# Optimization experiments

Measured on AMD Instinct MI355X. Metric: run time of the kernel, lower is better.

The kernel has to match this reference:

```python
import jax, jax.numpy as jnp
import numpy as np

VOCAB = 100000
EMB = 100
HID = 100
CTX_LEN = 60          # must equal MAX_DESC_LEN for linear_1 to fit
FACT_LEN = 20
DESC_LEN = 60


def setup_inputs() -> dict:
    key = jax.random.key(0)
    ks = jax.random.split(key, 12)
    s = 0.05
    context = jax.random.randint(ks[0], (CTX_LEN, FACT_LEN), 1, VOCAB)
    fact_lengths = jax.random.randint(ks[1], (CTX_LEN,), 1, FACT_LEN)
    description = jax.random.randint(ks[2], (DESC_LEN,), 1, VOCAB)
    emb_ctx = jax.random.normal(ks[3], (VOCAB, EMB), jnp.float32) * s
    emb_ctx = emb_ctx.at[0].set(0.0)  # padding_idx=0
    emb_dec = jax.random.normal(ks[4], (VOCAB, EMB), jnp.float32) * s
    emb_dec = emb_dec.at[0].set(0.0)
    w1 = jax.random.normal(ks[5], (HID, CTX_LEN * HID), jnp.float32) * s
    b1 = jax.random.normal(ks[6], (HID,), jnp.float32) * s
    w_ih = jax.random.normal(ks[7], (3 * HID, EMB), jnp.float32) * s
    w_hh = jax.random.normal(ks[8], (3 * HID, HID), jnp.float32) * s
    b_ih = jax.random.normal(ks[9], (3 * HID,), jnp.float32) * s
    b_hh = jax.random.normal(ks[10], (3 * HID,), jnp.float32) * s
    w_out = jax.random.normal(ks[11], (VOCAB, HID), jnp.float32) * s
    b_out = jnp.zeros((VOCAB,), jnp.float32)
    return {"context": context, "fact_lengths": fact_lengths, "description": description,
            "emb_ctx": emb_ctx, "emb_dec": emb_dec, "w1": w1, "b1": b1,
            "w_ih": w_ih, "w_hh": w_hh, "b_ih": b_ih, "b_hh": b_hh,
            "w_out": w_out, "b_out": b_out}


def _forward(context, description, emb_ctx, emb_dec, w1, b1,
             w_ih, w_hh, b_ih, b_hh, w_out, b_out):
    # ---- InputModule: embed + positional fact encoder ----
    emb = emb_ctx[context]                       # [CTX_LEN, FACT_LEN, EMB]
    slen, elen = FACT_LEN, EMB
    s = jnp.arange(slen, dtype=jnp.float32) / (slen - 1)   # [slen]
    e = jnp.arange(elen, dtype=jnp.float32) / (elen - 1)   # [elen]
    l = 1.0 - s[:, None] - e[None, :] * (1.0 - 2.0 * s[:, None])  # [slen, elen]
    facts = jnp.sum(emb * l[None], axis=1)       # [CTX_LEN, EMB]

    # ---- initial decoder hidden from flattened facts ----
    h0 = facts.reshape(1, -1) @ w1.T + b1        # [1, HID]

    x0 = emb_dec[1][None, :]                     # SOS token embedding [1, EMB]

    def step(carry, tok):
        h, x = carry
        gi = x @ w_ih.T + b_ih                   # [1, 3H]
        gh = h @ w_hh.T + b_hh
        i_r, i_z, i_n = jnp.split(gi, 3, axis=-1)
        h_r, h_z, h_n = jnp.split(gh, 3, axis=-1)
        r = jax.nn.sigmoid(i_r + h_r)
        z = jax.nn.sigmoid(i_z + h_z)
        n = jnp.tanh(i_n + r * h_n)
        h_new = (1.0 - z) * n + z * h            # [1, HID]
        logits = h_new @ w_out.T + b_out         # [1, VOCAB]
        logp = jax.nn.log_softmax(logits, axis=-1)
        loss_t = -logp[0, tok]                   # NLLLoss, batch 1
        x_next = emb_dec[tok][None, :]           # teacher forcing
        return (h_new, x_next), loss_t

    (_, _), losses = jax.lax.scan(step, (h0, x0), description)
    return jnp.sum(losses).reshape(1)            # matches torch FloatTensor([.])


def reference(context, fact_lengths, description, emb_ctx, emb_dec, w1, b1,
              w_ih, w_hh, b_ih, b_hh, w_out, b_out):
    # fact_lengths is unused by the original forward (PositionalFactEncoder ignores it)
    return _forward(context, description, emb_ctx, emb_dec, w1, b1,
                    w_ih, w_hh, b_ih, b_hh, w_out, b_out)
```

## Files before the change

kernel.cpp:

```cpp
#include <hip/hip_runtime.h>
#include <hip/hip_bf16.h>
#include <math.h>

#define VOCAB 100000
#define EMB 100
#define HID 100
#define CTX_LEN 60
#define FACT_LEN 20
#define DESC_LEN 60

#define WS_FACTS 0
#define WS_X     6000
#define WS_H0    12000
#define WS_GI    12160
#define WS_H     30160
#define WS_MS    36864
#define NWAVES   1024

typedef __attribute__((ext_vector_type(8))) short short8;
typedef __attribute__((ext_vector_type(4))) float f32x4;

static __device__ __forceinline__ unsigned short f2bf(float f) {
    union { float f; unsigned u; } x; x.f = f;
    unsigned r = (x.u + 0x7FFFu + ((x.u >> 16) & 1u)) >> 16;
    return (unsigned short)r;
}

__global__ __launch_bounds__(128) void k1_prep(const int* __restrict__ context,
                                               const int* __restrict__ desc,
                                               const float* __restrict__ emb_ctx,
                                               const float* __restrict__ emb_dec,
                                               float* __restrict__ ws,
                                               float* __restrict__ out) {
    int b = blockIdx.x, tid = threadIdx.x;
    if (b < 60) {
        __shared__ int toks[20];
        if (tid < 20) toks[tid] = context[b * 20 + tid];
        __syncthreads();
        if (tid < 100) {
            float ef = tid * (1.f / 99.f);
            float acc = 0.f;
            #pragma unroll
            for (int s = 0; s < 20; s++) {
                float sf = s * (1.f / 19.f);
                float l = 1.f - sf - ef * (1.f - 2.f * sf);
                acc = fmaf(emb_ctx[toks[s] * 100 + tid], l, acc);
            }
            ws[WS_FACTS + b * 100 + tid] = acc;
        }
    } else {
        int t = b - 60;
        int tok = (t == 0) ? 1 : desc[t - 1];
        if (tid < 100) ws[WS_X + t * 100 + tid] = emb_dec[tok * 100 + tid];
        if (b == 60 && tid == 0) out[0] = 0.f;
    }
}

__global__ __launch_bounds__(320) void k2_h0_gi(const float* __restrict__ w1,
                                                const float* __restrict__ b1,
                                                const float* __restrict__ w_ih,
                                                const float* __restrict__ b_ih,
                                                float* __restrict__ ws) {
    int b = blockIdx.x, tid = threadIdx.x;
    if (b < 100) {
        __shared__ float red[320];
        const float* facts = ws + WS_FACTS;
        const float* wr = w1 + b * 6000;
        float p = 0.f;
        for (int k = tid; k < 6000; k += 320) p = fmaf(facts[k], wr[k], p);
        red[tid] = p; __syncthreads();
        if (tid < 64) red[tid] += red[256 + tid];
        __syncthreads();
        for (int st = 128; st > 0; st >>= 1) {
            if (tid < st) red[tid] += red[tid + st];
            __syncthreads();
        }
        if (tid == 0) ws[WS_H0 + b] = red[0] + b1[b];
    } else {
        int t = b - 100;
        __shared__ float xs[100];
        if (tid < 100) xs[tid] = ws[WS_X + t * 100 + tid];
        __syncthreads();
        if (tid < 300) {
            float p = b_ih[tid];
            const float* wr = w_ih + tid * 100;
            #pragma unroll 4
            for (int k = 0; k < 100; k++) p = fmaf(wr[k], xs[k], p);
            ws[WS_GI + t * 300 + tid] = p;
        }
    }
}

__global__ __launch_bounds__(320) void k3_gru(const float* __restrict__ w_hh,
                                              const float* __restrict__ b_hh,
                                              float* __restrict__ ws) {
    __shared__ __align__(16) float h_lds[128];
    __shared__ float gh_lds[304];
    const int j = threadIdx.x;
    float wreg[100];
    float bhh = 0.f;
    if (j < 300) {
        bhh = b_hh[j];
        #pragma unroll
        for (int k4 = 0; k4 < 25; k4++) {
            float4 v = *(const float4*)(w_hh + j * 100 + k4 * 4);
            wreg[k4 * 4 + 0] = v.x; wreg[k4 * 4 + 1] = v.y;
            wreg[k4 * 4 + 2] = v.z; wreg[k4 * 4 + 3] = v.w;
        }
    }
    float hreg = 0.f;
    if (j < 100) { hreg = ws[WS_H0 + j]; h_lds[j] = hreg; }
    __syncthreads();

    const float* gi = ws + WS_GI;
    float* H = ws + WS_H;
    for (int t = 0; t < 60; t++) {
        if (j < 300) {
            float acc = bhh;
            #pragma unroll
            for (int k4 = 0; k4 < 25; k4++) {
                float4 hv = *(const float4*)(h_lds + k4 * 4);
                acc = fmaf(wreg[k4 * 4 + 0], hv.x, acc);
                acc = fmaf(wreg[k4 * 4 + 1], hv.y, acc);
                acc = fmaf(wreg[k4 * 4 + 2], hv.z, acc);
                acc = fmaf(wreg[k4 * 4 + 3], hv.w, acc);
            }
            gh_lds[j] = acc;
        }
        __syncthreads();
        if (j < 100) {
            float gir = gi[t * 300 + j];
            float giz = gi[t * 300 + 100 + j];
            float gin = gi[t * 300 + 200 + j];
            float ghr = gh_lds[j], ghz = gh_lds[100 + j], ghn = gh_lds[200 + j];
            float r = 1.f / (1.f + __expf(-(gir + ghr)));
            float z = 1.f / (1.f + __expf(-(giz + ghz)));
            float n = tanhf(fmaf(r, ghn, gin));
            hreg = (1.f - z) * n + z * hreg;
            h_lds[j] = hreg;
            H[t * 100 + j] = hreg;
        }
        __syncthreads();
    }
}

__global__ __launch_bounds__(256) void k4_logits(const float* __restrict__ w_out,
                                                 const float* __restrict__ b_out,
                                                 float* __restrict__ ws) {
    const float* H = ws + WS_H;
    float* ms = ws + WS_MS;
    const int lane = threadIdx.x & 63;
    const int gw = blockIdx.x * 4 + (threadIdx.x >> 6);
    const int q = lane >> 4, n = lane & 15;

    short8 afr[4][4];
    #pragma unroll
    for (int mt = 0; mt < 4; mt++) {
        int m = mt * 16 + n;
        #pragma unroll
        for (int kt = 0; kt < 4; kt++) {
            int k0 = kt * 32 + q * 8;
            short8 f;
            #pragma unroll
            for (int jj = 0; jj < 8; jj++) {
                float v = (m < 60 && (k0 + jj) < 100) ? H[m * 100 + k0 + jj] : 0.f;
                f[jj] = (short)f2bf(v);
            }
            afr[mt][kt] = f;
        }
    }

    float mS[16], sS[16];
    #pragma unroll
    for (int i = 0; i < 16; i++) { mS[i] = -3.0e38f; sS[i] = 0.f; }

    for (int c = gw; c < VOCAB / 16; c += NWAVES) {
        int row = c * 16 + n;
        short8 bfr[4];
        #pragma unroll
        for (int kt = 0; kt < 4; kt++) {
            int k0 = kt * 32 + q * 8;
            float va[8];
            if (k0 < 96) {
                float4 a = *(const float4*)(w_out + row * 100 + k0);
                float4 b = *(const float4*)(w_out + row * 100 + k0 + 4);
                va[0] = a.x; va[1] = a.y; va[2] = a.z; va[3] = a.w;
                va[4] = b.x; va[5] = b.y; va[6] = b.z; va[7] = b.w;
            } else if (k0 == 96) {
                float4 a = *(const float4*)(w_out + row * 100 + 96);
                va[0] = a.x; va[1] = a.y; va[2] = a.z; va[3] = a.w;
                va[4] = va[5] = va[6] = va[7] = 0.f;
            } else {
                #pragma unroll
                for (int jj = 0; jj < 8; jj++) va[jj] = 0.f;
            }
            short8 f;
            #pragma unroll
            for (int jj = 0; jj < 8; jj++) f[jj] = (short)f2bf(va[jj]);
            bfr[kt] = f;
        }
        float bo = b_out[row];
        #pragma unroll
        for (int mt = 0; mt < 4; mt++) {
            f32x4 acc = {0.f, 0.f, 0.f, 0.f};
            acc = __builtin_amdgcn_mfma_f32_16x16x32_bf16(afr[mt][0], bfr[0], acc, 0, 0, 0);
            acc = __builtin_amdgcn_mfma_f32_16x16x32_bf16(afr[mt][1], bfr[1], acc, 0, 0, 0);
            acc = __builtin_amdgcn_mfma_f32_16x16x32_bf16(afr[mt][2], bfr[2], acc, 0, 0, 0);
            acc = __builtin_amdgcn_mfma_f32_16x16x32_bf16(afr[mt][3], bfr[3], acc, 0, 0, 0);
            #pragma unroll
            for (int reg = 0; reg < 4; reg++) {
                float x = acc[reg] + bo;
                int i = mt * 4 + reg;
                float mo = mS[i];
                float mn = fmaxf(mo, x);
                sS[i] = sS[i] * __expf(mo - mn) + __expf(x - mn);
                mS[i] = mn;
            }
        }
    }

    #pragma unroll
    for (int i = 0; i < 16; i++) {
        float m = mS[i], s = sS[i];
        #pragma unroll
        for (int off = 1; off < 16; off <<= 1) {
            float m2 = __shfl_xor(m, off);
            float s2 = __shfl_xor(s, off);
            float mn = fmaxf(m, m2);
            s = s * __expf(m - mn) + s2 * __expf(m2 - mn);
            m = mn;
        }
        mS[i] = m; sS[i] = s;
    }
    if (n == 0) {
        #pragma unroll
        for (int mt = 0; mt < 4; mt++) {
            #pragma unroll
            for (int reg = 0; reg < 4; reg++) {
                int t = mt * 16 + q * 4 + reg;
                int i = mt * 4 + reg;
                float2 val; val.x = mS[i]; val.y = sS[i];
                ((float2*)ms)[t * NWAVES + gw] = val;
            }
        }
    }
}

__global__ __launch_bounds__(256) void k5_final(const int* __restrict__ desc,
                                                const float* __restrict__ w_out,
                                                const float* __restrict__ b_out,
                                                const float* __restrict__ ws,
                                                float* __restrict__ out) {
    int t = blockIdx.x, tid = threadIdx.x;
    __shared__ float sm[256], ss[256], sd[256];
    const float2* ms = (const float2*)(ws + WS_MS);
    float m = -3.0e38f, s = 0.f;
    for (int i = tid; i < NWAVES; i += 256) {
        float2 p = ms[t * NWAVES + i];
        float mn = fmaxf(m, p.x);
        s = s * __expf(m - mn) + p.y * __expf(p.x - mn);
        m = mn;
    }
    sm[tid] = m; ss[tid] = s; __syncthreads();
    for (int st = 128; st > 0; st >>= 1) {
        if (tid < st) {
            float mo = sm[tid], so = ss[tid];
            float m2 = sm[tid + st], s2 = ss[tid + st];
            float mn = fmaxf(mo, m2);
            sm[tid] = mn;
            ss[tid] = so * __expf(mo - mn) + s2 * __expf(m2 - mn);
        }
        __syncthreads();
    }
    int tok = desc[t];
    float p = 0.f;
    if (tid < 100) p = ws[WS_H + t * 100 + tid] * w_out[tok * 100 + tid];
    sd[tid] = p; __syncthreads();
    for (int st = 128; st > 0; st >>= 1) {
        if (tid < st) sd[tid] += sd[tid + st];
        __syncthreads();
    }
    if (tid == 0) {
        float logit = sd[0] + b_out[tok];
        float loss = sm[0] + logf(ss[0]) - logit;
        atomicAdd(out, loss);
    }
}

extern "C" void kernel_launch(void* const* d_in, const int* in_sizes, int n_in,
                              void* d_out, int out_size, void* d_ws, size_t ws_size,
                              hipStream_t stream) {
    const int*   context = (const int*)d_in[0];
    const int*   desc    = (const int*)d_in[2];
    const float* emb_ctx = (const float*)d_in[3];
    const float* emb_dec = (const float*)d_in[4];
    const float* w1      = (const float*)d_in[5];
    const float* b1      = (const float*)d_in[6];
    const float* w_ih    = (const float*)d_in[7];
    const float* w_hh    = (const float*)d_in[8];
    const float* b_ih    = (const float*)d_in[9];
    const float* b_hh    = (const float*)d_in[10];
    const float* w_out   = (const float*)d_in[11];
    const float* b_out   = (const float*)d_in[12];
    float* out = (float*)d_out;
    float* ws  = (float*)d_ws;

    k1_prep  <<<120, 128, 0, stream>>>(context, desc, emb_ctx, emb_dec, ws, out);
    k2_h0_gi <<<160, 320, 0, stream>>>(w1, b1, w_ih, b_ih, ws);
    k3_gru   <<<1,   320, 0, stream>>>(w_hh, b_hh, ws);
    k4_logits<<<256, 256, 0, stream>>>(w_out, b_out, ws);
    k5_final <<<60,  256, 0, stream>>>(desc, w_out, b_out, ws, out);
}
```

Baseline: 225.4 us.

## Double logits grid, split GRU FMA chains, fast tanh, vectorize H loads

The logits kernel now launches 512 blocks instead of 256 when the workspace is large enough, with the wave count passed at runtime to both the logits and final-reduction kernels. The GRU recurrence splits its dot product into four independent accumulators to shorten the serial FMA dependency chain, and replaces tanhf with an exp-based formula. H fragment loads become float4 vector loads, and the w_out load branches are simplified. The extra partial results raise the reduction work in k5, and the fast tanh plus reordered sums change rounding slightly.

```diff
diff --git a/kernel.cpp b/kernel.cpp
--- a/kernel.cpp
+++ b/kernel.cpp
@@ -8,6 +8,7 @@
 #define CTX_LEN 60
 #define FACT_LEN 20
 #define DESC_LEN 60
+#define NCHUNK (VOCAB / 16)
 
 #define WS_FACTS 0
 #define WS_X     6000
@@ -15,7 +16,6 @@
 #define WS_GI    12160
 #define WS_H     30160
 #define WS_MS    36864
-#define NWAVES   1024
 
 typedef __attribute__((ext_vector_type(8))) short short8;
 typedef __attribute__((ext_vector_type(4))) float f32x4;
@@ -91,9 +91,9 @@
     }
 }
 
-__global__ __launch_bounds__(320) void k3_gru(const float* __restrict__ w_hh,
-                                              const float* __restrict__ b_hh,
-                                              float* __restrict__ ws) {
+__global__ __launch_bounds__(320, 1) void k3_gru(const float* __restrict__ w_hh,
+                                                 const float* __restrict__ b_hh,
+                                                 float* __restrict__ ws) {
     __shared__ __align__(16) float h_lds[128];
     __shared__ float gh_lds[304];
     const int j = threadIdx.x;
@@ -116,16 +116,16 @@
     float* H = ws + WS_H;
     for (int t = 0; t < 60; t++) {
         if (j < 300) {
-            float acc = bhh;
+            float a0 = bhh, a1 = 0.f, a2 = 0.f, a3 = 0.f;
             #pragma unroll
             for (int k4 = 0; k4 < 25; k4++) {
                 float4 hv = *(const float4*)(h_lds + k4 * 4);
-                acc = fmaf(wreg[k4 * 4 + 0], hv.x, acc);
-                acc = fmaf(wreg[k4 * 4 + 1], hv.y, acc);
-                acc = fmaf(wreg[k4 * 4 + 2], hv.z, acc);
-                acc = fmaf(wreg[k4 * 4 + 3], hv.w, acc);
-            }
-            gh_lds[j] = acc;
+                a0 = fmaf(wreg[k4 * 4 + 0], hv.x, a0);
+                a1 = fmaf(wreg[k4 * 4 + 1], hv.y, a1);
+                a2 = fmaf(wreg[k4 * 4 + 2], hv.z, a2);
+                a3 = fmaf(wreg[k4 * 4 + 3], hv.w, a3);
+            }
+            gh_lds[j] = (a0 + a1) + (a2 + a3);
         }
         __syncthreads();
         if (j < 100) {
@@ -135,7 +135,9 @@
             float ghr = gh_lds[j], ghz = gh_lds[100 + j], ghn = gh_lds[200 + j];
             float r = 1.f / (1.f + __expf(-(gir + ghr)));
             float z = 1.f / (1.f + __expf(-(giz + ghz)));
-            float n = tanhf(fmaf(r, ghn, gin));
+            float a = fmaf(r, ghn, gin);
+            float tt = __expf(-2.f * fabsf(a));
+            float n = copysignf((1.f - tt) / (1.f + tt), a);
             hreg = (1.f - z) * n + z * hreg;
             h_lds[j] = hreg;
             H[t * 100 + j] = hreg;
@@ -144,14 +146,16 @@
     }
 }
 
-__global__ __launch_bounds__(256) void k4_logits(const float* __restrict__ w_out,
-                                                 const float* __restrict__ b_out,
-                                                 float* __restrict__ ws) {
+__global__ __launch_bounds__(256, 1) void k4_logits(const float* __restrict__ w_out,
+                                                    const float* __restrict__ b_out,
+                                                    float* __restrict__ ws,
+                                                    int nwaves) {
     const float* H = ws + WS_H;
     float* ms = ws + WS_MS;
     const int lane = threadIdx.x & 63;
     const int gw = blockIdx.x * 4 + (threadIdx.x >> 6);
     const int q = lane >> 4, n = lane & 15;
+    const int k_base = q * 8;
 
     short8 afr[4][4];
     #pragma unroll
@@ -159,13 +163,23 @@
         int m = mt * 16 + n;
         #pragma unroll
         for (int kt = 0; kt < 4; kt++) {
-            int k0 = kt * 32 + q * 8;
+            int k0 = kt * 32 + k_base;
+            float va[8];
+            #pragma unroll
+            for (int jj = 0; jj < 8; jj++) va[jj] = 0.f;
+            if (m < 60) {
+                if (k0 + 4 <= 100) {
+                    float4 a = *(const float4*)(H + m * 100 + k0);
+                    va[0] = a.x; va[1] = a.y; va[2] = a.z; va[3] = a.w;
+                }
+                if (k0 + 8 <= 100) {
+                    float4 b = *(const float4*)(H + m * 100 + k0 + 4);
+                    va[4] = b.x; va[5] = b.y; va[6] = b.z; va[7] = b.w;
+                }
+            }
             short8 f;
             #pragma unroll
-            for (int jj = 0; jj < 8; jj++) {
-                float v = (m < 60 && (k0 + jj) < 100) ? H[m * 100 + k0 + jj] : 0.f;
-                f[jj] = (short)f2bf(v);
-            }
+            for (int jj = 0; jj < 8; jj++) f[jj] = (short)f2bf(va[jj]);
             afr[mt][kt] = f;
         }
     }
@@ -174,25 +188,22 @@
     #pragma unroll
     for (int i = 0; i < 16; i++) { mS[i] = -3.0e38f; sS[i] = 0.f; }
 
-    for (int c = gw; c < VOCAB / 16; c += NWAVES) {
+    for (int c = gw; c < NCHUNK; c += nwaves) {
         int row = c * 16 + n;
         short8 bfr[4];
         #pragma unroll
         for (int kt = 0; kt < 4; kt++) {
-            int k0 = kt * 32 + q * 8;
+            int k0 = kt * 32 + k_base;
             float va[8];
-            if (k0 < 96) {
+            #pragma unroll
+            for (int jj = 0; jj < 8; jj++) va[jj] = 0.f;
+            if (k0 + 4 <= 100) {
                 float4 a = *(const float4*)(w_out + row * 100 + k0);
+                va[0] = a.x; va[1] = a.y; va[2] = a.z; va[3] = a.w;
+            }
+            if (k0 + 8 <= 100) {
                 float4 b = *(const float4*)(w_out + row * 100 + k0 + 4);
-                va[0] = a.x; va[1] = a.y; va[2] = a.z; va[3] = a.w;
                 va[4] = b.x; va[5] = b.y; va[6] = b.z; va[7] = b.w;
-            } else if (k0 == 96) {
-                float4 a = *(const float4*)(w_out + row * 100 + 96);
-                va[0] = a.x; va[1] = a.y; va[2] = a.z; va[3] = a.w;
-                va[4] = va[5] = va[6] = va[7] = 0.f;
-            } else {
-                #pragma unroll
-                for (int jj = 0; jj < 8; jj++) va[jj] = 0.f;
             }
             short8 f;
             #pragma unroll
@@ -239,8 +250,10 @@
             for (int reg = 0; reg < 4; reg++) {
                 int t = mt * 16 + q * 4 + reg;
                 int i = mt * 4 + reg;
-                float2 val; val.x = mS[i]; val.y = sS[i];
-                ((float2*)ms)[t * NWAVES + gw] = val;
+                if (t < 60) {
+                    float2 val; val.x = mS[i]; val.y = sS[i];
+                    ((float2*)ms)[t * nwaves + gw] = val;
+                }
             }
         }
     }
@@ -250,13 +263,14 @@
                                                 const float* __restrict__ w_out,
                                                 const float* __restrict__ b_out,
                                                 const float* __restrict__ ws,
-                                                float* __restrict__ out) {
+                                                float* __restrict__ out,
+                                                int nwaves) {
     int t = blockIdx.x, tid = threadIdx.x;
     __shared__ float sm[256], ss[256], sd[256];
     const float2* ms = (const float2*)(ws + WS_MS);
     float m = -3.0e38f, s = 0.f;
-    for (int i = tid; i < NWAVES; i += 256) {
-        float2 p = ms[t * NWAVES + i];
+    for (int i = tid; i < nwaves; i += 256) {
+        float2 p = ms[t * nwaves + i];
         float mn = fmaxf(m, p.x);
         s = s * __expf(m - mn) + p.y * __expf(p.x - mn);
         m = mn;
@@ -305,9 +319,14 @@
     float* out = (float*)d_out;
     float* ws  = (float*)d_ws;
 
+    int nblocks = 512;
+    size_t need = (size_t)(WS_MS + 60 * (nblocks * 4) * 2) * 4;
+    if (ws_size < need) nblocks = 256;
+    int nwaves = nblocks * 4;
+
     k1_prep  <<<120, 128, 0, stream>>>(context, desc, emb_ctx, emb_dec, ws, out);
     k2_h0_gi <<<160, 320, 0, stream>>>(w1, b1, w_ih, b_ih, ws);
     k3_gru   <<<1,   320, 0, stream>>>(w_hh, b_hh, ws);
-    k4_logits<<<256, 256, 0, stream>>>(w_out, b_out, ws);
-    k5_final <<<60,  256, 0, stream>>>(desc, w_out, b_out, ws, out);
-}
+    k4_logits<<<nblocks, 256, 0, stream>>>(w_out, b_out, ws, nwaves);
+    k5_final <<<60,  256, 0, stream>>>(desc, w_out, b_out, ws, out, nwaves);
+}
```

After: 248.1 us. +10.1%, slower.
